# Kernel optimization log

Measured on AMD Instinct MI355X. Metric: run time of the kernel, lower is better.

The kernel has to match this reference:

```python
import jax, jax.numpy as jnp
import numpy as np

K_DIM = 768
HEADS = 8
HEAD_DIM = K_DIM // HEADS  # 96


def setup_inputs() -> dict:
    key = jax.random.key(0)
    ks = jax.random.split(key, 6)
    b, t = 4, 2048
    scale = 1.0 / np.sqrt(HEAD_DIM)
    return {
        "input_x": jax.random.normal(ks[0], (b, t, K_DIM), dtype=jnp.float32),
        "Wq": jax.random.normal(ks[1], (HEAD_DIM, HEAD_DIM), dtype=jnp.float32) * scale,
        "Wk": jax.random.normal(ks[2], (HEAD_DIM, HEAD_DIM), dtype=jnp.float32) * scale,
        "Wv": jax.random.normal(ks[3], (HEAD_DIM, HEAD_DIM), dtype=jnp.float32) * scale,
        "Wu": jax.random.normal(ks[4], (K_DIM, K_DIM), dtype=jnp.float32) * (1.0 / np.sqrt(K_DIM)),
        "bu": jax.random.normal(ks[5], (K_DIM,), dtype=jnp.float32) * 0.01,
    }


def reference(input_x, Wq, Wk, Wv, Wu, bu):
    b, t, k = input_x.shape
    h, d = HEADS, k // HEADS
    # split into heads: [b, t, h, d]; per-head projections share the same d x d weights
    x = input_x.reshape(b, t, h, d)
    inv4 = 1.0 / (k ** 0.25)
    q = jnp.einsum("bthd,od->btho", x, Wq) * inv4  # scaled queries
    kk = jnp.einsum("bthd,od->btho", x, Wk) * inv4  # scaled keys
    v = jnp.einsum("bthd,od->btho", x, Wv)
    # full attention matrix [b, h, t, t] (materialized, as in the original bmm impl)
    scores = jnp.einsum("bthd,bshd->bhts", q, kk)
    attn = jax.nn.softmax(scores, axis=-1)
    out = jnp.einsum("bhts,bshd->bthd", attn, v).reshape(b, t, k)
    return out @ Wu.T + bu
```

## Files before the change

kernel.cpp:

```cpp
#include <hip/hip_runtime.h>
#include <hip/hip_bf16.h>
#include <math.h>

#define TB 2048
#define NB 4
#define NH 8
#define HD 96
#define KD 768

typedef unsigned short u16;
typedef __attribute__((ext_vector_type(4))) u16 u16x4;
typedef __attribute__((ext_vector_type(8))) u16 u16x8;
typedef __attribute__((ext_vector_type(4))) float f32x4;
typedef __attribute__((ext_vector_type(16))) float f32x16;
typedef __attribute__((ext_vector_type(4))) unsigned u32x4;
typedef __attribute__((ext_vector_type(8))) __bf16 bf16x8;

__device__ __forceinline__ u16 f2bf(float f) {
    unsigned u = __builtin_bit_cast(unsigned, f);
    u += 0x7FFFu + ((u >> 16) & 1u);
    return (u16)(u >> 16);
}
__device__ __forceinline__ bf16x8 cast8(u16x8 u) { return __builtin_bit_cast(bf16x8, u); }
__device__ __forceinline__ unsigned pkbf(float a, float b) {
    unsigned w;
    asm("v_cvt_pk_bf16_f32 %0, %1, %2" : "=v"(w) : "v"(a), "v"(b));
    return w;
}

__global__ __launch_bounds__(256) void qkv_proj(
    const float* __restrict__ x, const float* __restrict__ Wq,
    const float* __restrict__ Wk, const float* __restrict__ Wv,
    u16* __restrict__ Q, u16* __restrict__ Kout, u16* __restrict__ VT, float inv4)
{
    __shared__ __align__(16) u16 Wl[3][96][104];
    __shared__ __align__(16) u16 Rp[96 * 72];
    const int tid = threadIdx.x;
    for (int idx = tid; idx < 3 * 9216; idx += 256) {
        int m = idx / 9216, rem = idx % 9216;
        const float* Wsrc = (m == 0) ? Wq : (m == 1) ? Wk : Wv;
        float scale = (m < 2) ? inv4 : 1.0f;
        int r = rem / 96, c = rem % 96;
        Wl[m][r][c] = f2bf(Wsrc[rem] * scale);
    }
    __syncthreads();

    const int w = tid >> 6, l = tid & 63;
    const int lc = l & 15, lk = l >> 4;
    const int bh = blockIdx.y, b = bh >> 3, h = bh & 7;
    const int t0 = blockIdx.x * 64;
    const int tw = t0 + w * 16;

    bf16x8 afrag[3];
    {
        const float* xp = x + ((long)((b * TB + tw + lc) * NH + h)) * HD + 8 * lk;
#pragma unroll
        for (int c = 0; c < 3; ++c) {
            f32x4 f0 = *(const f32x4*)(xp + c * 32);
            f32x4 f1 = *(const f32x4*)(xp + c * 32 + 4);
            u16x8 u;
#pragma unroll
            for (int j = 0; j < 4; ++j) { u[j] = f2bf(f0[j]); u[4 + j] = f2bf(f1[j]); }
            afrag[c] = cast8(u);
        }
    }

    const f32x4 Z4 = {0.f, 0.f, 0.f, 0.f};
    u16* outs[2] = {Q, Kout};
#pragma unroll
    for (int m = 0; m < 2; ++m) {
        f32x4 acc[6];
#pragma unroll
        for (int nt = 0; nt < 6; ++nt) acc[nt] = Z4;
#pragma unroll
        for (int c = 0; c < 3; ++c) {
#pragma unroll
            for (int nt = 0; nt < 6; ++nt) {
                u16x8 bw = *(const u16x8*)&Wl[m][nt * 16 + lc][c * 32 + 8 * lk];
                acc[nt] = __builtin_amdgcn_mfma_f32_16x16x32_bf16(afrag[c], cast8(bw), acc[nt], 0, 0, 0);
            }
        }
        __syncthreads();
#pragma unroll
        for (int nt = 0; nt < 6; ++nt)
#pragma unroll
            for (int reg = 0; reg < 4; ++reg)
                Rp[(w * 16 + lk * 4 + reg) * 104 + nt * 16 + lc] = f2bf(acc[nt][reg]);
        __syncthreads();
#pragma unroll
        for (int ci = 0; ci < 3; ++ci) {
            int ch = tid + ci * 256;
            int row = ch / 12, cc = (ch % 12) * 8;
            *(u16x8*)(outs[m] + ((long)bh * TB + t0 + row) * HD + cc) = *(const u16x8*)&Rp[row * 104 + cc];
        }
    }
    {
        f32x4 acc[6];
#pragma unroll
        for (int nt = 0; nt < 6; ++nt) acc[nt] = Z4;
#pragma unroll
        for (int c = 0; c < 3; ++c) {
#pragma unroll
            for (int nt = 0; nt < 6; ++nt) {
                u16x8 aw = *(const u16x8*)&Wl[2][nt * 16 + lc][c * 32 + 8 * lk];
                acc[nt] = __builtin_amdgcn_mfma_f32_16x16x32_bf16(cast8(aw), afrag[c], acc[nt], 0, 0, 0);
            }
        }
        __syncthreads();
#pragma unroll
        for (int nt = 0; nt < 6; ++nt)
#pragma unroll
            for (int reg = 0; reg < 4; ++reg) {
                int o = nt * 16 + lk * 4 + reg;
                Rp[o * 72 + w * 16 + lc] = f2bf(acc[nt][reg]);
            }
        __syncthreads();
#pragma unroll
        for (int ci = 0; ci < 3; ++ci) {
            int ch = tid + ci * 256;
            int row = ch >> 3, tc = (ch & 7) * 8;
            *(u16x8*)(VT + ((long)bh * HD + row) * TB + t0 + tc) = *(const u16x8*)&Rp[row * 72 + tc];
        }
    }
}

#define KVB 32
#define VOFF2 (KVB * 104)
#define SLAB2 (KVB * 104 + 96 * 40)

__global__ __launch_bounds__(256) void attn(
    const u16* __restrict__ Q, const u16* __restrict__ Kin, const u16* __restrict__ VT,
    u16* __restrict__ O)
{
    __shared__ __align__(16) u16 SM[2][SLAB2];

    const int tid = threadIdx.x;
    const int w = tid >> 6, l = tid & 63;
    const int m32 = l & 31, hi = l >> 5;
    const int lid = (blockIdx.x & 7) * 32 + (blockIdx.x >> 3);
    const int qt = lid & 7, bh = lid >> 3;
    const int q0 = qt * 256 + w * 64;

    const u16* Qb = Q + (long)bh * TB * HD;
    const u16* Kb = Kin + (long)bh * TB * HD;
    const u16* Vb = VT + (long)bh * HD * TB;

    const u16* gbase[3]; int loff[3]; int mult[3];
#pragma unroll
    for (int ci = 0; ci < 3; ++ci) {
        int ch = tid + ci * 256;
        if (ch < 384) {
            int row = ch / 12, cc = (ch % 12) * 8;
            gbase[ci] = Kb + row * HD + cc;
            mult[ci] = HD;
            loff[ci] = row * 104 + cc;
        } else {
            int c2 = ch - 384;
            int d = c2 >> 2, sc = (c2 & 3) * 8;
            gbase[ci] = Vb + (long)d * TB + sc;
            mult[ci] = 1;
            loff[ci] = VOFF2 + d * 40 + sc;
        }
    }

    bf16x8 qb[2][6];
#pragma unroll
    for (int qs = 0; qs < 2; ++qs)
#pragma unroll
        for (int kk = 0; kk < 6; ++kk)
            qb[qs][kk] = cast8(*(const u16x8*)(Qb + (long)(q0 + qs * 32 + m32) * HD + kk * 16 + 8 * hi));

    u16x8 r[3];
#pragma unroll
    for (int ci = 0; ci < 3; ++ci) r[ci] = *(const u16x8*)(gbase[ci]);
#pragma unroll
    for (int ci = 0; ci < 3; ++ci) *(u16x8*)(SM[0] + loff[ci]) = r[ci];
#pragma unroll
    for (int ci = 0; ci < 3; ++ci) r[ci] = *(const u16x8*)(gbase[ci] + (long)KVB * mult[ci]);

    float m_st[2] = {-1e30f, -1e30f}, l_st[2] = {0.f, 0.f};
    f32x16 accO[3][2];
#pragma unroll
    for (int dt = 0; dt < 3; ++dt)
#pragma unroll
        for (int qs = 0; qs < 2; ++qs)
#pragma unroll
            for (int rr = 0; rr < 16; ++rr) accO[dt][qs][rr] = 0.f;

    const int NST = TB / KVB;
    for (int st = 0; st < NST; ++st) {
        __syncthreads();
        if (st < NST - 1) {
            u16* dst = SM[(st + 1) & 1];
#pragma unroll
            for (int ci = 0; ci < 3; ++ci) *(u16x8*)(dst + loff[ci]) = r[ci];
            int s2 = (st + 2 < NST ? st + 2 : NST - 1) * KVB;
#pragma unroll
            for (int ci = 0; ci < 3; ++ci) r[ci] = *(const u16x8*)(gbase[ci] + (long)s2 * mult[ci]);
        }
        const u16* KP = SM[st & 1];
        const u16* VP = SM[st & 1] + VOFF2;

        f32x16 sa[2];
#pragma unroll
        for (int qs = 0; qs < 2; ++qs)
#pragma unroll
            for (int rr = 0; rr < 16; ++rr) sa[qs][rr] = 0.f;
        __builtin_amdgcn_s_setprio(1);
#pragma unroll
        for (int kk = 0; kk < 6; ++kk) {
            u16x8 kf = *(const u16x8*)(KP + m32 * 104 + kk * 16 + 8 * hi);
            sa[0] = __builtin_amdgcn_mfma_f32_32x32x16_bf16(cast8(kf), qb[0][kk], sa[0], 0, 0, 0);
            sa[1] = __builtin_amdgcn_mfma_f32_32x32x16_bf16(cast8(kf), qb[1][kk], sa[1], 0, 0, 0);
        }
        __builtin_amdgcn_s_setprio(0);

        float tm[2];
#pragma unroll
        for (int qs = 0; qs < 2; ++qs) {
            float t2 = sa[qs][0];
#pragma unroll
            for (int rr = 1; rr < 16; ++rr) t2 = fmaxf(t2, sa[qs][rr]);
            t2 = fmaxf(t2, __shfl_xor(t2, 32));
            tm[qs] = t2;
        }
        if (!__all(tm[0] - m_st[0] <= 8.0f && tm[1] - m_st[1] <= 8.0f)) {
#pragma unroll
            for (int qs = 0; qs < 2; ++qs) {
                float mnew = fmaxf(m_st[qs], tm[qs]);
                float alpha = __expf(m_st[qs] - mnew);
#pragma unroll
                for (int dt = 0; dt < 3; ++dt)
#pragma unroll
                    for (int rr = 0; rr < 16; ++rr) accO[dt][qs][rr] *= alpha;
                l_st[qs] *= alpha;
                m_st[qs] = mnew;
            }
        }
#pragma unroll
        for (int qs = 0; qs < 2; ++qs) {
            float sum = 0.f;
#pragma unroll
            for (int rr = 0; rr < 16; ++rr) {
                float pv = __expf(sa[qs][rr] - m_st[qs]);
                sa[qs][rr] = pv;
                sum += pv;
            }
            sum += __shfl_xor(sum, 32);
            l_st[qs] += sum;
        }

        bf16x8 pb0[2], pb1[2];
#pragma unroll
        for (int qs = 0; qs < 2; ++qs) {
            unsigned A1 = pkbf(sa[qs][0], sa[qs][1]);
            unsigned A2 = pkbf(sa[qs][2], sa[qs][3]);
            unsigned B1 = pkbf(sa[qs][4], sa[qs][5]);
            unsigned B2 = pkbf(sa[qs][6], sa[qs][7]);
            unsigned A3 = pkbf(sa[qs][8], sa[qs][9]);
            unsigned A4 = pkbf(sa[qs][10], sa[qs][11]);
            unsigned B3 = pkbf(sa[qs][12], sa[qs][13]);
            unsigned B4 = pkbf(sa[qs][14], sa[qs][15]);
            unsigned xA1 = __shfl_xor((int)A1, 32), xA2 = __shfl_xor((int)A2, 32);
            unsigned xB1 = __shfl_xor((int)B1, 32), xB2 = __shfl_xor((int)B2, 32);
            unsigned xA3 = __shfl_xor((int)A3, 32), xA4 = __shfl_xor((int)A4, 32);
            unsigned xB3 = __shfl_xor((int)B3, 32), xB4 = __shfl_xor((int)B4, 32);
            u32x4 t0v = { hi ? xB1 : A1, hi ? xB2 : A2, hi ? B1 : xA1, hi ? B2 : xA2 };
            u32x4 t1v = { hi ? xB3 : A3, hi ? xB4 : A4, hi ? B3 : xA3, hi ? B4 : xA4 };
            pb0[qs] = __builtin_bit_cast(bf16x8, t0v);
            pb1[qs] = __builtin_bit_cast(bf16x8, t1v);
        }

        __builtin_amdgcn_s_setprio(1);
#pragma unroll
        for (int dt = 0; dt < 3; ++dt) {
            u16x8 vf0 = *(const u16x8*)(VP + (dt * 32 + m32) * 40 + 8 * hi);
            accO[dt][0] = __builtin_amdgcn_mfma_f32_32x32x16_bf16(cast8(vf0), pb0[0], accO[dt][0], 0, 0, 0);
            accO[dt][1] = __builtin_amdgcn_mfma_f32_32x32x16_bf16(cast8(vf0), pb0[1], accO[dt][1], 0, 0, 0);
            u16x8 vf1 = *(const u16x8*)(VP + (dt * 32 + m32) * 40 + 16 + 8 * hi);
            accO[dt][0] = __builtin_amdgcn_mfma_f32_32x32x16_bf16(cast8(vf1), pb1[0], accO[dt][0], 0, 0, 0);
            accO[dt][1] = __builtin_amdgcn_mfma_f32_32x32x16_bf16(cast8(vf1), pb1[1], accO[dt][1], 0, 0, 0);
        }
        __builtin_amdgcn_s_setprio(0);
    }

    const int b = bh >> 3, h = bh & 7;
#pragma unroll
    for (int qs = 0; qs < 2; ++qs) {
        float linv = 1.0f / l_st[qs];
        int t = q0 + qs * 32 + m32;
        u16* op = O + ((long)(b * TB + t)) * KD + h * HD;
#pragma unroll
        for (int dt = 0; dt < 3; ++dt)
#pragma unroll
            for (int g = 0; g < 4; ++g) {
                u16x4 v = { f2bf(accO[dt][qs][g * 4 + 0] * linv), f2bf(accO[dt][qs][g * 4 + 1] * linv),
                            f2bf(accO[dt][qs][g * 4 + 2] * linv), f2bf(accO[dt][qs][g * 4 + 3] * linv) };
                *(u16x4*)(op + dt * 32 + g * 8 + 4 * hi) = v;
            }
    }
}

__global__ __launch_bounds__(256) void wu_conv(const float* __restrict__ Wu, u16* __restrict__ Wub) {
    int i = (blockIdx.x * 256 + threadIdx.x) * 4;
    f32x4 f = *(const f32x4*)(Wu + i);
    u16x4 o = { f2bf(f[0]), f2bf(f[1]), f2bf(f[2]), f2bf(f[3]) };
    *(u16x4*)(Wub + i) = o;
}

__global__ __launch_bounds__(256) void out_gemm(
    const u16* __restrict__ O, const u16* __restrict__ Wub,
    const float* __restrict__ bu, float* __restrict__ out)
{
    __shared__ __align__(16) u16 Al[2][128][68];
    __shared__ __align__(16) u16 Bl[2][128][68];
    const int tid = threadIdx.x;
    const int w = tid >> 6, l = tid & 63;
    const int m32 = l & 31, hi = l >> 5;
    const int wr = w >> 1, wc = w & 1;
    const int lid = (blockIdx.x & 7) * 48 + (blockIdx.x >> 3);
    const int nb = lid % 6, mb = lid / 6;
    const int m0 = mb * 128, n0 = nb * 128;

    const int crow = tid >> 3, ccol = (tid & 7) * 8;

    f32x16 acc[2][2];
#pragma unroll
    for (int i = 0; i < 2; ++i)
#pragma unroll
        for (int j = 0; j < 2; ++j)
#pragma unroll
            for (int rr = 0; rr < 16; ++rr) acc[i][j][rr] = 0.f;

    u16x8 ra[4], rb[4];
#pragma unroll
    for (int i = 0; i < 4; ++i) {
        ra[i] = *(const u16x8*)(O   + (long)(m0 + crow + i * 32) * KD + ccol);
        rb[i] = *(const u16x8*)(Wub + (long)(n0 + crow + i * 32) * KD + ccol);
    }
#pragma unroll
    for (int i = 0; i < 4; ++i) {
        *(u16x8*)&Al[0][crow + i * 32][ccol] = ra[i];
        *(u16x8*)&Bl[0][crow + i * 32][ccol] = rb[i];
    }
#pragma unroll
    for (int i = 0; i < 4; ++i) {
        ra[i] = *(const u16x8*)(O   + (long)(m0 + crow + i * 32) * KD + 64 + ccol);
        rb[i] = *(const u16x8*)(Wub + (long)(n0 + crow + i * 32) * KD + 64 + ccol);
    }

    for (int kt = 0; kt < KD / 64; ++kt) {
        __syncthreads();
        if (kt < KD / 64 - 1) {
            int p = (kt + 1) & 1;
#pragma unroll
            for (int i = 0; i < 4; ++i) {
                *(u16x8*)&Al[p][crow + i * 32][ccol] = ra[i];
                *(u16x8*)&Bl[p][crow + i * 32][ccol] = rb[i];
            }
            int cn = (kt + 2 < KD / 64 ? kt + 2 : KD / 64 - 1) * 64;
#pragma unroll
            for (int i = 0; i < 4; ++i) {
                ra[i] = *(const u16x8*)(O   + (long)(m0 + crow + i * 32) * KD + cn + ccol);
                rb[i] = *(const u16x8*)(Wub + (long)(n0 + crow + i * 32) * KD + cn + ccol);
            }
        }
        int p = kt & 1;
        __builtin_amdgcn_s_setprio(1);
#pragma unroll
        for (int k16 = 0; k16 < 4; ++k16) {
            bf16x8 afr[2], bfr[2];
#pragma unroll
            for (int rb2 = 0; rb2 < 2; ++rb2)
                afr[rb2] = cast8(*(const u16x8*)&Al[p][wr * 64 + rb2 * 32 + m32][k16 * 16 + 8 * hi]);
#pragma unroll
            for (int cb2 = 0; cb2 < 2; ++cb2)
                bfr[cb2] = cast8(*(const u16x8*)&Bl[p][wc * 64 + cb2 * 32 + m32][k16 * 16 + 8 * hi]);
#pragma unroll
            for (int rb2 = 0; rb2 < 2; ++rb2)
#pragma unroll
                for (int cb2 = 0; cb2 < 2; ++cb2)
                    acc[rb2][cb2] = __builtin_amdgcn_mfma_f32_32x32x16_bf16(afr[rb2], bfr[cb2], acc[rb2][cb2], 0, 0, 0);
        }
        __builtin_amdgcn_s_setprio(0);
    }

    const float bv0 = bu[n0 + wc * 64 + m32];
    const float bv1 = bu[n0 + wc * 64 + 32 + m32];
#pragma unroll
    for (int rb2 = 0; rb2 < 2; ++rb2)
#pragma unroll
        for (int cb2 = 0; cb2 < 2; ++cb2) {
            float bv = cb2 ? bv1 : bv0;
            int nn = n0 + wc * 64 + cb2 * 32 + m32;
#pragma unroll
            for (int reg = 0; reg < 16; ++reg) {
                int mm = m0 + wr * 64 + rb2 * 32 + (reg & 3) + 8 * (reg >> 2) + 4 * hi;
                out[(long)mm * KD + nn] = acc[rb2][cb2][reg] + bv;
            }
        }
}

extern "C" void kernel_launch(void* const* d_in, const int* in_sizes, int n_in,
                              void* d_out, int out_size, void* d_ws, size_t ws_size,
                              hipStream_t stream) {
    const float* x  = (const float*)d_in[0];
    const float* Wq = (const float*)d_in[1];
    const float* Wk = (const float*)d_in[2];
    const float* Wv = (const float*)d_in[3];
    const float* Wu = (const float*)d_in[4];
    const float* bu = (const float*)d_in[5];
    float* out = (float*)d_out;

    u16* ws = (u16*)d_ws;
    const size_t SZ = (size_t)NB * NH * TB * HD;
    u16* Q   = ws;
    u16* Kq  = ws + SZ;
    u16* VT  = ws + 2 * SZ;
    u16* O   = ws + 3 * SZ;
    u16* Wub = ws;

    const float inv4 = 1.0f / powf((float)KD, 0.25f);

    qkv_proj<<<dim3(TB / 64, NB * NH), dim3(256), 0, stream>>>(x, Wq, Wk, Wv, Q, Kq, VT, inv4);
    attn<<<dim3(TB / 256 * NB * NH), dim3(256), 0, stream>>>(Q, Kq, VT, O);
    wu_conv<<<dim3((KD * KD) / 1024), dim3(256), 0, stream>>>(Wu, Wub);
    out_gemm<<<dim3((NB * TB / 128) * (KD / 128)), dim3(256), 0, stream>>>(O, Wub, bu, out);
}
```

Before: 232.2 us.

## Split attention KV range across two wave groups and pre-convert QKV weights

```diff
diff --git a/kernel.cpp b/kernel.cpp
--- a/kernel.cpp
+++ b/kernel.cpp
@@ -28,20 +28,35 @@
     return w;
 }
 
+__global__ __launch_bounds__(256) void w_conv(
+    const float* __restrict__ Wq, const float* __restrict__ Wk,
+    const float* __restrict__ Wv, u16* __restrict__ Wb, float inv4)
+{
+    int i = (blockIdx.x * 256 + threadIdx.x) * 4;
+    const float* src; float sc; int off;
+    if (i < 9216)       { src = Wq; off = i;         sc = inv4; }
+    else if (i < 18432) { src = Wk; off = i - 9216;  sc = inv4; }
+    else                { src = Wv; off = i - 18432; sc = 1.0f; }
+    f32x4 f = *(const f32x4*)(src + off);
+    u16x4 o = { f2bf(f[0] * sc), f2bf(f[1] * sc), f2bf(f[2] * sc), f2bf(f[3] * sc) };
+    *(u16x4*)(Wb + i) = o;
+}
+
 __global__ __launch_bounds__(256) void qkv_proj(
-    const float* __restrict__ x, const float* __restrict__ Wq,
-    const float* __restrict__ Wk, const float* __restrict__ Wv,
-    u16* __restrict__ Q, u16* __restrict__ Kout, u16* __restrict__ VT, float inv4)
+    const float* __restrict__ x, const u16* __restrict__ Wb,
+    u16* __restrict__ Q, u16* __restrict__ Kout, u16* __restrict__ VT)
 {
     __shared__ __align__(16) u16 Wl[3][96][104];
     __shared__ __align__(16) u16 Rp[96 * 72];
     const int tid = threadIdx.x;
-    for (int idx = tid; idx < 3 * 9216; idx += 256) {
-        int m = idx / 9216, rem = idx % 9216;
-        const float* Wsrc = (m == 0) ? Wq : (m == 1) ? Wk : Wv;
-        float scale = (m < 2) ? inv4 : 1.0f;
-        int r = rem / 96, c = rem % 96;
-        Wl[m][r][c] = f2bf(Wsrc[rem] * scale);
+#pragma unroll
+    for (int ci = 0; ci < 14; ++ci) {
+        int ch = tid + ci * 256;
+        if (ch < 3456) {
+            int m = ch / 1152, rem = ch % 1152;
+            int rr = rem / 12, cc = (rem % 12) * 8;
+            *(u16x8*)&Wl[m][rr][cc] = *(const u16x8*)(Wb + m * 9216 + rr * 96 + cc);
+        }
     }
     __syncthreads();
 
@@ -124,42 +139,44 @@
     }
 }
 
-#define KVB 32
-#define VOFF2 (KVB * 104)
-#define SLAB2 (KVB * 104 + 96 * 40)
-
-__global__ __launch_bounds__(256) void attn(
+#define KVB 64
+#define VOFFA (KVB * 104)
+#define SLABA (KVB * 104 + HD * 72)
+
+__global__ __launch_bounds__(512, 2) void attn(
     const u16* __restrict__ Q, const u16* __restrict__ Kin, const u16* __restrict__ VT,
     u16* __restrict__ O)
 {
-    __shared__ __align__(16) u16 SM[2][SLAB2];
+    __shared__ __align__(16) u16 SM[2][2][SLABA];
 
     const int tid = threadIdx.x;
     const int w = tid >> 6, l = tid & 63;
     const int m32 = l & 31, hi = l >> 5;
+    const int g = w >> 2, w2 = w & 3;
     const int lid = (blockIdx.x & 7) * 32 + (blockIdx.x >> 3);
     const int qt = lid & 7, bh = lid >> 3;
-    const int q0 = qt * 256 + w * 64;
+    const int q0 = qt * 256 + w2 * 64;
 
     const u16* Qb = Q + (long)bh * TB * HD;
     const u16* Kb = Kin + (long)bh * TB * HD;
     const u16* Vb = VT + (long)bh * HD * TB;
 
-    const u16* gbase[3]; int loff[3]; int mult[3];
-#pragma unroll
-    for (int ci = 0; ci < 3; ++ci) {
-        int ch = tid + ci * 256;
-        if (ch < 384) {
+    const int ltid = tid & 255;
+    const u16* gbase[6]; int loff[6]; int mult[6];
+#pragma unroll
+    for (int ci = 0; ci < 6; ++ci) {
+        int ch = ltid + ci * 256;
+        if (ch < 768) {
             int row = ch / 12, cc = (ch % 12) * 8;
-            gbase[ci] = Kb + row * HD + cc;
+            gbase[ci] = Kb + ((long)g * 1024 + row) * HD + cc;
             mult[ci] = HD;
             loff[ci] = row * 104 + cc;
         } else {
-            int c2 = ch - 384;
-            int d = c2 >> 2, sc = (c2 & 3) * 8;
-            gbase[ci] = Vb + (long)d * TB + sc;
+            int c2 = ch - 768;
+            int d = c2 >> 3, sc = (c2 & 7) * 8;
+            gbase[ci] = Vb + (long)d * TB + g * 1024 + sc;
             mult[ci] = 1;
-            loff[ci] = VOFF2 + d * 40 + sc;
+            loff[ci] = VOFFA + d * 72 + sc;
         }
     }
 
@@ -170,13 +187,13 @@
         for (int kk = 0; kk < 6; ++kk)
             qb[qs][kk] = cast8(*(const u16x8*)(Qb + (long)(q0 + qs * 32 + m32) * HD + kk * 16 + 8 * hi));
 
-    u16x8 r[3];
-#pragma unroll
-    for (int ci = 0; ci < 3; ++ci) r[ci] = *(const u16x8*)(gbase[ci]);
-#pragma unroll
-    for (int ci = 0; ci < 3; ++ci) *(u16x8*)(SM[0] + loff[ci]) = r[ci];
-#pragma unroll
-    for (int ci = 0; ci < 3; ++ci) r[ci] = *(const u16x8*)(gbase[ci] + (long)KVB * mult[ci]);
+    u16x8 r[6];
+#pragma unroll
+    for (int ci = 0; ci < 6; ++ci) r[ci] = *(const u16x8*)(gbase[ci]);
+#pragma unroll
+    for (int ci = 0; ci < 6; ++ci) *(u16x8*)(&SM[g][0][0] + loff[ci]) = r[ci];
+#pragma unroll
+    for (int ci = 0; ci < 6; ++ci) r[ci] = *(const u16x8*)(gbase[ci] + (long)KVB * mult[ci]);
 
     float m_st[2] = {-1e30f, -1e30f}, l_st[2] = {0.f, 0.f};
     f32x16 accO[3][2];
@@ -187,117 +204,159 @@
 #pragma unroll
             for (int rr = 0; rr < 16; ++rr) accO[dt][qs][rr] = 0.f;
 
-    const int NST = TB / KVB;
+    const int NST = 1024 / KVB;
     for (int st = 0; st < NST; ++st) {
         __syncthreads();
         if (st < NST - 1) {
-            u16* dst = SM[(st + 1) & 1];
-#pragma unroll
-            for (int ci = 0; ci < 3; ++ci) *(u16x8*)(dst + loff[ci]) = r[ci];
+            u16* dst = &SM[g][(st + 1) & 1][0];
+#pragma unroll
+            for (int ci = 0; ci < 6; ++ci) *(u16x8*)(dst + loff[ci]) = r[ci];
             int s2 = (st + 2 < NST ? st + 2 : NST - 1) * KVB;
 #pragma unroll
-            for (int ci = 0; ci < 3; ++ci) r[ci] = *(const u16x8*)(gbase[ci] + (long)s2 * mult[ci]);
-        }
-        const u16* KP = SM[st & 1];
-        const u16* VP = SM[st & 1] + VOFF2;
-
-        f32x16 sa[2];
-#pragma unroll
-        for (int qs = 0; qs < 2; ++qs)
-#pragma unroll
-            for (int rr = 0; rr < 16; ++rr) sa[qs][rr] = 0.f;
-        __builtin_amdgcn_s_setprio(1);
-#pragma unroll
-        for (int kk = 0; kk < 6; ++kk) {
-            u16x8 kf = *(const u16x8*)(KP + m32 * 104 + kk * 16 + 8 * hi);
-            sa[0] = __builtin_amdgcn_mfma_f32_32x32x16_bf16(cast8(kf), qb[0][kk], sa[0], 0, 0, 0);
-            sa[1] = __builtin_amdgcn_mfma_f32_32x32x16_bf16(cast8(kf), qb[1][kk], sa[1], 0, 0, 0);
-        }
-        __builtin_amdgcn_s_setprio(0);
-
-        float tm[2];
+            for (int ci = 0; ci < 6; ++ci) r[ci] = *(const u16x8*)(gbase[ci] + (long)s2 * mult[ci]);
+        }
+        const u16* KP = &SM[g][st & 1][0];
+        const u16* VP = KP + VOFFA;
+
+#pragma unroll
+        for (int sub = 0; sub < 2; ++sub) {
+            f32x16 sa[2];
+#pragma unroll
+            for (int qs = 0; qs < 2; ++qs)
+#pragma unroll
+                for (int rr = 0; rr < 16; ++rr) sa[qs][rr] = 0.f;
+            __builtin_amdgcn_s_setprio(1);
+#pragma unroll
+            for (int kk = 0; kk < 6; ++kk) {
+                u16x8 kf = *(const u16x8*)(KP + (sub * 32 + m32) * 104 + kk * 16 + 8 * hi);
+                sa[0] = __builtin_amdgcn_mfma_f32_32x32x16_bf16(cast8(kf), qb[0][kk], sa[0], 0, 0, 0);
+                sa[1] = __builtin_amdgcn_mfma_f32_32x32x16_bf16(cast8(kf), qb[1][kk], sa[1], 0, 0, 0);
+            }
+            __builtin_amdgcn_s_setprio(0);
+
+            float tm[2];
+#pragma unroll
+            for (int qs = 0; qs < 2; ++qs) {
+                float t2 = sa[qs][0];
+#pragma unroll
+                for (int rr = 1; rr < 16; ++rr) t2 = fmaxf(t2, sa[qs][rr]);
+                t2 = fmaxf(t2, __shfl_xor(t2, 32));
+                tm[qs] = t2;
+            }
+            if (!__all(tm[0] - m_st[0] <= 8.0f && tm[1] - m_st[1] <= 8.0f)) {
+#pragma unroll
+                for (int qs = 0; qs < 2; ++qs) {
+                    float mnew = fmaxf(m_st[qs], tm[qs]);
+                    float alpha = __expf(m_st[qs] - mnew);
+#pragma unroll
+                    for (int dt = 0; dt < 3; ++dt)
+#pragma unroll
+                        for (int rr = 0; rr < 16; ++rr) accO[dt][qs][rr] *= alpha;
+                    l_st[qs] *= alpha;
+                    m_st[qs] = mnew;
+                }
+            }
+#pragma unroll
+            for (int qs = 0; qs < 2; ++qs) {
+                float sum = 0.f;
+#pragma unroll
+                for (int rr = 0; rr < 16; ++rr) {
+                    float pv = __expf(sa[qs][rr] - m_st[qs]);
+                    sa[qs][rr] = pv;
+                    sum += pv;
+                }
+                sum += __shfl_xor(sum, 32);
+                l_st[qs] += sum;
+            }
+
+            bf16x8 pb0[2], pb1[2];
+#pragma unroll
+            for (int qs = 0; qs < 2; ++qs) {
+                unsigned A1 = pkbf(sa[qs][0], sa[qs][1]);
+                unsigned A2 = pkbf(sa[qs][2], sa[qs][3]);
+                unsigned B1 = pkbf(sa[qs][4], sa[qs][5]);
+                unsigned B2 = pkbf(sa[qs][6], sa[qs][7]);
+                unsigned A3 = pkbf(sa[qs][8], sa[qs][9]);
+                unsigned A4 = pkbf(sa[qs][10], sa[qs][11]);
+                unsigned B3 = pkbf(sa[qs][12], sa[qs][13]);
+                unsigned B4 = pkbf(sa[qs][14], sa[qs][15]);
+                unsigned xA1 = __shfl_xor((int)A1, 32), xA2 = __shfl_xor((int)A2, 32);
+                unsigned xB1 = __shfl_xor((int)B1, 32), xB2 = __shfl_xor((int)B2, 32);
+                unsigned xA3 = __shfl_xor((int)A3, 32), xA4 = __shfl_xor((int)A4, 32);
+                unsigned xB3 = __shfl_xor((int)B3, 32), xB4 = __shfl_xor((int)B4, 32);
+                u32x4 t0v = { hi ? xB1 : A1, hi ? xB2 : A2, hi ? B1 : xA1, hi ? B2 : xA2 };
+                u32x4 t1v = { hi ? xB3 : A3, hi ? xB4 : A4, hi ? B3 : xA3, hi ? B4 : xA4 };
+                pb0[qs] = __builtin_bit_cast(bf16x8, t0v);
+                pb1[qs] = __builtin_bit_cast(bf16x8, t1v);
+            }
+
+            __builtin_amdgcn_s_setprio(1);
+#pragma unroll
+            for (int dt = 0; dt < 3; ++dt) {
+                u16x8 vf0 = *(const u16x8*)(VP + (dt * 32 + m32) * 72 + sub * 32 + 8 * hi);
+                accO[dt][0] = __builtin_amdgcn_mfma_f32_32x32x16_bf16(cast8(vf0), pb0[0], accO[dt][0], 0, 0, 0);
+                accO[dt][1] = __builtin_amdgcn_mfma_f32_32x32x16_bf16(cast8(vf0), pb0[1], accO[dt][1], 0, 0, 0);
+                u16x8 vf1 = *(const u16x8*)(VP + (dt * 32 + m32) * 72 + sub * 32 + 16 + 8 * hi);
+                accO[dt][0] = __builtin_amdgcn_mfma_f32_32x32x16_bf16(cast8(vf1), pb1[0], accO[dt][0], 0, 0, 0);
+                accO[dt][1] = __builtin_amdgcn_mfma_f32_32x32x16_bf16(cast8(vf1), pb1[1], accO[dt][1], 0, 0, 0);
+            }
+            __builtin_amdgcn_s_setprio(0);
+        }
+    }
+
+    float* MB = (float*)&SM[0][0][0];
+    float* LB = MB + 1024;
+    float* OB = MB + 2048;
+    {
+        int mi = ((g * 4 + w2) * 2) * 64 + l;
+        MB[mi] = m_st[0]; MB[mi + 64] = m_st[1];
+        LB[mi] = l_st[0]; LB[mi + 64] = l_st[1];
+    }
+    __syncthreads();
+    float a_self[2], l_tot[2];
+    {
+        int pi = (((g ^ 1) * 4 + w2) * 2) * 64 + l;
 #pragma unroll
         for (int qs = 0; qs < 2; ++qs) {
-            float t2 = sa[qs][0];
-#pragma unroll
-            for (int rr = 1; rr < 16; ++rr) t2 = fmaxf(t2, sa[qs][rr]);
-            t2 = fmaxf(t2, __shfl_xor(t2, 32));
-            tm[qs] = t2;
-        }
-        if (!__all(tm[0] - m_st[0] <= 8.0f && tm[1] - m_st[1] <= 8.0f)) {
-#pragma unroll
-            for (int qs = 0; qs < 2; ++qs) {
-                float mnew = fmaxf(m_st[qs], tm[qs]);
-                float alpha = __expf(m_st[qs] - mnew);
-#pragma unroll
-                for (int dt = 0; dt < 3; ++dt)
-#pragma unroll
-                    for (int rr = 0; rr < 16; ++rr) accO[dt][qs][rr] *= alpha;
-                l_st[qs] *= alpha;
-                m_st[qs] = mnew;
-            }
-        }
+            float mo = MB[pi + qs * 64], lo = LB[pi + qs * 64];
+            float mx = fmaxf(m_st[qs], mo);
+            a_self[qs] = __expf(m_st[qs] - mx);
+            float ao = __expf(mo - mx);
+            l_tot[qs] = a_self[qs] * l_st[qs] + ao * lo;
+        }
+    }
+    if (g == 1) {
+        float* ob = OB + (w2 * 64 + l) * 97;
+#pragma unroll
+        for (int dt = 0; dt < 3; ++dt)
+#pragma unroll
+            for (int qs = 0; qs < 2; ++qs)
+#pragma unroll
+                for (int rr = 0; rr < 16; ++rr)
+                    ob[(dt * 2 + qs) * 16 + rr] = accO[dt][qs][rr] * a_self[qs];
+    }
+    __syncthreads();
+    if (g == 0) {
+        const int b = bh >> 3, h = bh & 7;
+        const float* ob = OB + (w2 * 64 + l) * 97;
 #pragma unroll
         for (int qs = 0; qs < 2; ++qs) {
-            float sum = 0.f;
-#pragma unroll
-            for (int rr = 0; rr < 16; ++rr) {
-                float pv = __expf(sa[qs][rr] - m_st[qs]);
-                sa[qs][rr] = pv;
-                sum += pv;
-            }
-            sum += __shfl_xor(sum, 32);
-            l_st[qs] += sum;
-        }
-
-        bf16x8 pb0[2], pb1[2];
-#pragma unroll
-        for (int qs = 0; qs < 2; ++qs) {
-            unsigned A1 = pkbf(sa[qs][0], sa[qs][1]);
-            unsigned A2 = pkbf(sa[qs][2], sa[qs][3]);
-            unsigned B1 = pkbf(sa[qs][4], sa[qs][5]);
-            unsigned B2 = pkbf(sa[qs][6], sa[qs][7]);
-            unsigned A3 = pkbf(sa[qs][8], sa[qs][9]);
-            unsigned A4 = pkbf(sa[qs][10], sa[qs][11]);
-            unsigned B3 = pkbf(sa[qs][12], sa[qs][13]);
-            unsigned B4 = pkbf(sa[qs][14], sa[qs][15]);
-            unsigned xA1 = __shfl_xor((int)A1, 32), xA2 = __shfl_xor((int)A2, 32);
-            unsigned xB1 = __shfl_xor((int)B1, 32), xB2 = __shfl_xor((int)B2, 32);
-            unsigned xA3 = __shfl_xor((int)A3, 32), xA4 = __shfl_xor((int)A4, 32);
-            unsigned xB3 = __shfl_xor((int)B3, 32), xB4 = __shfl_xor((int)B4, 32);
-            u32x4 t0v = { hi ? xB1 : A1, hi ? xB2 : A2, hi ? B1 : xA1, hi ? B2 : xA2 };
-            u32x4 t1v = { hi ? xB3 : A3, hi ? xB4 : A4, hi ? B3 : xA3, hi ? B4 : xA4 };
-            pb0[qs] = __builtin_bit_cast(bf16x8, t0v);
-            pb1[qs] = __builtin_bit_cast(bf16x8, t1v);
-        }
-
-        __builtin_amdgcn_s_setprio(1);
-#pragma unroll
-        for (int dt = 0; dt < 3; ++dt) {
-            u16x8 vf0 = *(const u16x8*)(VP + (dt * 32 + m32) * 40 + 8 * hi);
-            accO[dt][0] = __builtin_amdgcn_mfma_f32_32x32x16_bf16(cast8(vf0), pb0[0], accO[dt][0], 0, 0, 0);
-            accO[dt][1] = __builtin_amdgcn_mfma_f32_32x32x16_bf16(cast8(vf0), pb0[1], accO[dt][1], 0, 0, 0);
-            u16x8 vf1 = *(const u16x8*)(VP + (dt * 32 + m32) * 40 + 16 + 8 * hi);
-            accO[dt][0] = __builtin_amdgcn_mfma_f32_32x32x16_bf16(cast8(vf1), pb1[0], accO[dt][0], 0, 0, 0);
-            accO[dt][1] = __builtin_amdgcn_mfma_f32_32x32x16_bf16(cast8(vf1), pb1[1], accO[dt][1], 0, 0, 0);
-        }
-        __builtin_amdgcn_s_setprio(0);
-    }
-
-    const int b = bh >> 3, h = bh & 7;
-#pragma unroll
-    for (int qs = 0; qs < 2; ++qs) {
-        float linv = 1.0f / l_st[qs];
-        int t = q0 + qs * 32 + m32;
-        u16* op = O + ((long)(b * TB + t)) * KD + h * HD;
-#pragma unroll
-        for (int dt = 0; dt < 3; ++dt)
-#pragma unroll
-            for (int g = 0; g < 4; ++g) {
-                u16x4 v = { f2bf(accO[dt][qs][g * 4 + 0] * linv), f2bf(accO[dt][qs][g * 4 + 1] * linv),
-                            f2bf(accO[dt][qs][g * 4 + 2] * linv), f2bf(accO[dt][qs][g * 4 + 3] * linv) };
-                *(u16x4*)(op + dt * 32 + g * 8 + 4 * hi) = v;
-            }
+            float linv = 1.0f / l_tot[qs];
+            int t = q0 + qs * 32 + m32;
+            u16* op = O + ((long)(b * TB + t)) * KD + h * HD;
+#pragma unroll
+            for (int dt = 0; dt < 3; ++dt)
+#pragma unroll
+                for (int g4 = 0; g4 < 4; ++g4) {
+                    u16x4 v;
+#pragma unroll
+                    for (int j = 0; j < 4; ++j) {
+                        float pv = accO[dt][qs][g4 * 4 + j] * a_self[qs] + ob[(dt * 2 + qs) * 16 + g4 * 4 + j];
+                        v[j] = f2bf(pv * linv);
+                    }
+                    *(u16x4*)(op + dt * 32 + g4 * 8 + 4 * hi) = v;
+                }
+        }
     }
 }
 
@@ -419,11 +478,13 @@
     u16* VT  = ws + 2 * SZ;
     u16* O   = ws + 3 * SZ;
     u16* Wub = ws;
+    u16* Wb  = (u16*)d_out;
 
     const float inv4 = 1.0f / powf((float)KD, 0.25f);
 
-    qkv_proj<<<dim3(TB / 64, NB * NH), dim3(256), 0, stream>>>(x, Wq, Wk, Wv, Q, Kq, VT, inv4);
-    attn<<<dim3(TB / 256 * NB * NH), dim3(256), 0, stream>>>(Q, Kq, VT, O);
+    w_conv<<<dim3(27), dim3(256), 0, stream>>>(Wq, Wk, Wv, Wb, inv4);
+    qkv_proj<<<dim3(TB / 64, NB * NH), dim3(256), 0, stream>>>(x, Wb, Q, Kq, VT);
+    attn<<<dim3(TB / 256 * NB * NH), dim3(512), 0, stream>>>(Q, Kq, VT, O);
     wu_conv<<<dim3((KD * KD) / 1024), dim3(256), 0, stream>>>(Wu, Wub);
     out_gemm<<<dim3((NB * TB / 128) * (KD / 128)), dim3(256), 0, stream>>>(O, Wub, bu, out);
 }
```

After: 186.4 us. 1.25x faster.
